# Performance work log

Hardware: AMD Instinct MI355X
Metric: run time of the kernel (lower is better)

Reference implementation:

```python
import jax, jax.numpy as jnp
import numpy as np

B, N, C_IN, C_OUT, CHEB_K, EMBED = 64, 2048, 64, 64, 3, 16


def setup_inputs() -> dict:
    key = jax.random.key(0)
    k1, k2, k3, k4 = jax.random.split(key, 4)
    return {
        "graph": 0,  # unused placeholder, matches original signature
        "node_feature": jax.random.normal(k1, (B, N, C_IN), dtype=jnp.float32),
        "node_embeddings": jax.random.normal(k2, (N, EMBED), dtype=jnp.float32),
        "weights_pool": jax.random.normal(k3, (EMBED, CHEB_K, C_IN, C_OUT), dtype=jnp.float32),
        "bias_pool": jax.random.normal(k4, (EMBED, C_OUT), dtype=jnp.float32),
    }


def reference(graph, node_feature, node_embeddings, weights_pool, bias_pool):
    x = node_feature                      # [B, N, C]
    n = node_embeddings.shape[0]
    # adaptive adjacency: softmax(relu(E E^T)) row-wise
    supports = jax.nn.softmax(jax.nn.relu(node_embeddings @ node_embeddings.T), axis=1)  # [N, N]
    # Chebyshev polynomial basis
    support_set = [jnp.eye(n, dtype=supports.dtype), supports]
    for _ in range(2, CHEB_K):
        support_set.append(2.0 * supports @ support_set[-1] - support_set[-2])
    supports_k = jnp.stack(support_set, axis=0)  # [K, N, N]
    # per-node dynamic weights / bias
    weights = jnp.einsum('nd,dkio->nkio', node_embeddings, weights_pool)  # [N, K, I, O]
    bias = node_embeddings @ bias_pool                                    # [N, O]
    # graph aggregation over Chebyshev orders
    x_g = jnp.einsum('knm,bmc->bnkc', supports_k, x)                      # [B, N, K, C]
    # per-node weighted contraction
    out = jnp.einsum('bnki,nkio->bno', x_g, weights) + bias               # [B, N, O]
    return out
```

## Files before the change

kernel.cpp:

```cpp
#include <hip/hip_runtime.h>
#include <hip/hip_bf16.h>

#define BB 64
#define NN 2048
#define CC 64
#define DD 16

typedef __attribute__((ext_vector_type(8))) short bf16x8;
typedef __attribute__((ext_vector_type(4))) float f32x4;

__device__ __forceinline__ ushort f2bf(float f) {
  unsigned u = __float_as_uint(f);
  u += 0x7fffu + ((u >> 16) & 1u);
  return (ushort)(u >> 16);
}
__device__ __forceinline__ float b2f(ushort h) {
  return __uint_as_float(((unsigned)h) << 16);
}

#define GLOAD16(g, l)                                                 \
  __builtin_amdgcn_global_load_lds(                                   \
      (const __attribute__((address_space(1))) void*)(g),             \
      (__attribute__((address_space(3))) void*)(l), 16, 0, 0)

__global__ __launch_bounds__(256) void transpose_x_kernel(
    const float* __restrict__ X, ushort* __restrict__ Xt) {
  const int b = blockIdx.y;
  const int m0 = blockIdx.x * 256;
  const int t = threadIdx.x;
  __shared__ ushort xs[256 * 64];

#pragma unroll
  for (int it = 0; it < 16; ++it) {
    const int idx = it * 256 + t;
    const int m = idx >> 4;
    const int cq = (idx & 15) * 4;
    float4 v = *(const float4*)&X[(size_t)b * NN * CC + (size_t)(m0 + m) * CC + cq];
    ushort4 h;
    h.x = f2bf(v.x); h.y = f2bf(v.y); h.z = f2bf(v.z); h.w = f2bf(v.w);
    *(ushort4*)((char*)xs + m * 128 + ((cq * 2) ^ ((m & 7) << 4))) = h;
  }
  __syncthreads();

  const int c = t >> 2;
  const int mb = (t & 3) * 64;
#pragma unroll
  for (int s = 0; s < 8; ++s) {
    unsigned w0 = 0, w1 = 0, w2 = 0, w3 = 0;
#pragma unroll
    for (int j = 0; j < 8; ++j) {
      const int m = mb + s * 8 + j;
      const ushort hv =
          *(const ushort*)((const char*)xs + m * 128 + ((2 * c) ^ ((m & 7) << 4)));
      const unsigned uv = (unsigned)hv << ((j & 1) * 16);
      if (j < 2) w0 |= uv; else if (j < 4) w1 |= uv;
      else if (j < 6) w2 |= uv; else w3 |= uv;
    }
    uint4 pk = {w0, w1, w2, w3};
    *(uint4*)&Xt[(size_t)b * CC * NN + (size_t)c * NN + m0 + mb + s * 8] = pk;
  }
}

__global__ __launch_bounds__(256) void wpt_kernel(
    const float* __restrict__ Wp, ushort* __restrict__ Wpt) {
  const int g = blockIdx.x * 256 + threadIdx.x;
  const int d = g / 1536;
  const int rem = g % 1536;
  const int o = rem / 24;
  const int ki0 = (rem % 24) * 8;
  bf16x8 h;
#pragma unroll
  for (int j = 0; j < 8; ++j)
    h[j] = (short)f2bf(Wp[d * 12288 + (ki0 + j) * 64 + o]);
  *(bf16x8*)&Wpt[d * 12288 + o * 192 + ki0] = h;
}

__global__ __launch_bounds__(256) void supports_kernel(
    const float* __restrict__ E, ushort* __restrict__ S) {
  const int n = blockIdx.x;
  const int t = threadIdx.x;

  __shared__ float en[DD];
  if (t < DD) en[t] = E[n * DD + t];
  __syncthreads();

  float e[DD];
#pragma unroll
  for (int d = 0; d < DD; ++d) e[d] = en[d];

  float vals[8];
  float vmax = 0.f;
#pragma unroll
  for (int j = 0; j < 8; ++j) {
    const int m = j * 256 + t;
    const float4* Em = (const float4*)&E[m * DD];
    float4 v0 = Em[0], v1 = Em[1], v2 = Em[2], v3 = Em[3];
    float dot = e[0]*v0.x + e[1]*v0.y + e[2]*v0.z + e[3]*v0.w
              + e[4]*v1.x + e[5]*v1.y + e[6]*v1.z + e[7]*v1.w
              + e[8]*v2.x + e[9]*v2.y + e[10]*v2.z + e[11]*v2.w
              + e[12]*v3.x + e[13]*v3.y + e[14]*v3.z + e[15]*v3.w;
    dot = fmaxf(dot, 0.f);
    vals[j] = dot;
    vmax = fmaxf(vmax, dot);
  }

  __shared__ float red[256];
  red[t] = vmax;
  __syncthreads();
  for (int s = 128; s > 0; s >>= 1) {
    if (t < s) red[t] = fmaxf(red[t], red[t + s]);
    __syncthreads();
  }
  vmax = red[0];
  __syncthreads();

  float sum = 0.f;
#pragma unroll
  for (int j = 0; j < 8; ++j) {
    vals[j] = __expf(vals[j] - vmax);
    sum += vals[j];
  }
  red[t] = sum;
  __syncthreads();
  for (int s = 128; s > 0; s >>= 1) {
    if (t < s) red[t] += red[t + s];
    __syncthreads();
  }
  const float inv = 1.f / red[0];

#pragma unroll
  for (int j = 0; j < 8; ++j)
    S[(size_t)n * NN + j * 256 + t] = f2bf(vals[j] * inv);
}

__global__ __launch_bounds__(256) void spmm_t_kernel(
    const ushort* __restrict__ At, const ushort* __restrict__ S,
    ushort* __restrict__ Yt, ushort* __restrict__ Yn) {
  const int b  = blockIdx.x;
  const int n0 = blockIdx.y * 256;
  const int t  = threadIdx.x;
  const int w  = t >> 6;
  const int l  = t & 63;

  __shared__ ushort Als[64 * 64];
  __shared__ ushort Bls[256 * 64];

  const char* Abase = (const char*)(At + (size_t)b * CC * NN);
  const char* Sbase = (const char*)S + (size_t)n0 * (NN * 2);

  f32x4 acc[4][4];
#pragma unroll
  for (int i = 0; i < 4; ++i)
#pragma unroll
    for (int j = 0; j < 4; ++j) acc[i][j] = (f32x4)0.f;

  const int lkb = (l & 7) * 16;
  const int lrw = w * 8 + (l >> 3);

  for (int mt = 0; mt < NN; mt += 64) {
    __syncthreads();
#pragma unroll
    for (int q = 0; q < 2; ++q) {
      const int row = q * 32 + lrw;
      GLOAD16(Abase + (size_t)row * (NN * 2) + mt * 2 + (lkb ^ ((row & 7) << 4)),
              (char*)Als + q * 4096 + w * 1024);
    }
#pragma unroll
    for (int q = 0; q < 8; ++q) {
      const int row = q * 32 + lrw;
      GLOAD16(Sbase + (size_t)row * (NN * 2) + mt * 2 + (lkb ^ ((row & 7) << 4)),
              (char*)Bls + q * 4096 + w * 1024);
    }
    __syncthreads();

#pragma unroll
    for (int kk = 0; kk < 2; ++kk) {
      const int kb = kk * 64 + (l >> 4) * 16;
      bf16x8 a[4], bv[4];
#pragma unroll
      for (int cf = 0; cf < 4; ++cf) {
        const int c = cf * 16 + (l & 15);
        a[cf] = *(const bf16x8*)((const char*)Als + c * 128 + (kb ^ ((c & 7) << 4)));
      }
#pragma unroll
      for (int nf = 0; nf < 4; ++nf) {
        const int r = w * 64 + nf * 16 + (l & 15);
        bv[nf] = *(const bf16x8*)((const char*)Bls + r * 128 + (kb ^ ((r & 7) << 4)));
      }
#pragma unroll
      for (int cf = 0; cf < 4; ++cf)
#pragma unroll
        for (int nf = 0; nf < 4; ++nf)
          acc[cf][nf] = __builtin_amdgcn_mfma_f32_16x16x32_bf16(
              a[cf], bv[nf], acc[cf][nf], 0, 0, 0);
    }
  }

  const int nw = n0 + w * 64;
#pragma unroll
  for (int cf = 0; cf < 4; ++cf) {
#pragma unroll
    for (int nf = 0; nf < 4; ++nf) {
      const int n = nw + nf * 16 + (l & 15);
      const int cb = cf * 16 + (l >> 4) * 4;
      ushort h0 = f2bf(acc[cf][nf][0]);
      ushort h1 = f2bf(acc[cf][nf][1]);
      ushort h2 = f2bf(acc[cf][nf][2]);
      ushort h3 = f2bf(acc[cf][nf][3]);
      if (Yt) {
        ushort* p = Yt + (size_t)b * CC * NN + (size_t)cb * NN + n;
        p[0] = h0; p[NN] = h1; p[2 * NN] = h2; p[3 * NN] = h3;
      }
      if (Yn) {
        ushort4 pk = {h0, h1, h2, h3};
        *(ushort4*)(Yn + (size_t)b * NN * CC + (size_t)n * CC + cb) = pk;
      }
    }
  }
}

__global__ __launch_bounds__(256) void out_kernel(
    const float* __restrict__ E, const ushort* __restrict__ Wpt,
    const float* __restrict__ Bp, const float* __restrict__ X,
    const ushort* __restrict__ Y1n, const ushort* __restrict__ Y1t,
    const ushort* __restrict__ Y2n, float* __restrict__ Out) {
  const int n = blockIdx.x;
  const int t = threadIdx.x;
  const int w = t >> 6, l = t & 63;

  __shared__ ushort Wt[64 * 192];
  __shared__ ushort xg[64 * 192];
  __shared__ float bsh[64];
  __shared__ float esh[DD];

  if (t < DD) esh[t] = E[n * DD + t];
  __syncthreads();
  float e[DD];
#pragma unroll
  for (int d = 0; d < DD; ++d) e[d] = esh[d];

  if (t < 64) {
    float bsum = 0.f;
#pragma unroll
    for (int d = 0; d < DD; ++d) bsum = fmaf(e[d], Bp[d * 64 + t], bsum);
    bsh[t] = bsum;
  }

#pragma unroll
  for (int it = 0; it < 6; ++it) {
    const int boff = it * 4096 + t * 16;
    float acc[8] = {};
#pragma unroll
    for (int d = 0; d < DD; ++d) {
      bf16x8 wv = *(const bf16x8*)((const char*)Wpt + d * 24576 + boff);
#pragma unroll
      for (int u = 0; u < 8; ++u)
        acc[u] = fmaf(e[d], b2f((ushort)wv[u]), acc[u]);
    }
    bf16x8 hv;
#pragma unroll
    for (int u = 0; u < 8; ++u) hv[u] = (short)f2bf(acc[u]);
    const int o = boff / 384;
    const int kib = boff % 384;
    *(bf16x8*)((char*)Wt + o * 384 + (kib ^ ((o & 7) << 4))) = hv;
  }

  {
    const int b = t >> 2, i0 = (t & 3) * 16;
    const size_t NC = (size_t)NN * CC;
    const size_t gbase = (size_t)b * NC + (size_t)n * CC + i0;
    float xv[16];
#pragma unroll
    for (int j = 0; j < 4; ++j) {
      float4 v = *(const float4*)&X[gbase + j * 4];
      xv[j * 4 + 0] = v.x; xv[j * 4 + 1] = v.y;
      xv[j * 4 + 2] = v.z; xv[j * 4 + 3] = v.w;
    }
#pragma unroll
    for (int h = 0; h < 2; ++h) {
      bf16x8 hv;
#pragma unroll
      for (int u = 0; u < 8; ++u) hv[u] = (short)f2bf(xv[h * 8 + u]);
      const int ki = i0 + h * 8;
      *(bf16x8*)((char*)xg + b * 384 + ((ki * 2) ^ ((b & 7) << 4))) = hv;
    }
    if (Y1n) {
#pragma unroll
      for (int h = 0; h < 2; ++h) {
        bf16x8 hv = *(const bf16x8*)&Y1n[gbase + h * 8];
        const int ki = 64 + i0 + h * 8;
        *(bf16x8*)((char*)xg + b * 384 + ((ki * 2) ^ ((b & 7) << 4))) = hv;
      }
    } else {
#pragma unroll
      for (int h = 0; h < 2; ++h) {
        bf16x8 hv;
#pragma unroll
        for (int u = 0; u < 8; ++u)
          hv[u] = (short)Y1t[(size_t)b * NC + (size_t)(i0 + h * 8 + u) * NN + n];
        const int ki = 64 + i0 + h * 8;
        *(bf16x8*)((char*)xg + b * 384 + ((ki * 2) ^ ((b & 7) << 4))) = hv;
      }
    }
#pragma unroll
    for (int h = 0; h < 2; ++h) {
      bf16x8 y2 = *(const bf16x8*)&Y2n[gbase + h * 8];
      bf16x8 hv;
#pragma unroll
      for (int u = 0; u < 8; ++u)
        hv[u] = (short)f2bf(2.f * b2f((ushort)y2[u]) - xv[h * 8 + u]);
      const int ki = 128 + i0 + h * 8;
      *(bf16x8*)((char*)xg + b * 384 + ((ki * 2) ^ ((b & 7) << 4))) = hv;
    }
  }
  __syncthreads();

  const int br = (w & 1) * 32, oc = (w >> 1) * 32;
  f32x4 acc[2][2];
#pragma unroll
  for (int i = 0; i < 2; ++i)
#pragma unroll
    for (int j = 0; j < 2; ++j) acc[i][j] = (f32x4)0.f;

#pragma unroll
  for (int s = 0; s < 6; ++s) {
    const int kb = s * 64 + (l >> 4) * 16;
    bf16x8 av[2], bv[2];
#pragma unroll
    for (int i = 0; i < 2; ++i) {
      const int row = br + i * 16 + (l & 15);
      av[i] = *(const bf16x8*)((const char*)xg + row * 384 + (kb ^ ((row & 7) << 4)));
    }
#pragma unroll
    for (int j = 0; j < 2; ++j) {
      const int row = oc + j * 16 + (l & 15);
      bv[j] = *(const bf16x8*)((const char*)Wt + row * 384 + (kb ^ ((row & 7) << 4)));
    }
#pragma unroll
    for (int i = 0; i < 2; ++i)
#pragma unroll
      for (int j = 0; j < 2; ++j)
        acc[i][j] = __builtin_amdgcn_mfma_f32_16x16x32_bf16(av[i], bv[j],
                                                            acc[i][j], 0, 0, 0);
  }

  const size_t NC = (size_t)NN * CC;
#pragma unroll
  for (int i = 0; i < 2; ++i) {
#pragma unroll
    for (int j = 0; j < 2; ++j) {
      const int o = oc + j * 16 + (l & 15);
      const int bb = br + i * 16 + (l >> 4) * 4;
      const float bo = bsh[o];
#pragma unroll
      for (int r = 0; r < 4; ++r)
        Out[(size_t)(bb + r) * NC + (size_t)n * CC + o] = acc[i][j][r] + bo;
    }
  }
}

extern "C" void kernel_launch(void* const* d_in, const int* in_sizes, int n_in,
                              void* d_out, int out_size, void* d_ws, size_t ws_size,
                              hipStream_t stream) {
  const float* x  = (const float*)d_in[1];
  const float* E  = (const float*)d_in[2];
  const float* Wp = (const float*)d_in[3];
  const float* Bp = (const float*)d_in[4];
  float* out = (float*)d_out;

  const size_t szS  = (size_t)NN * NN * 2;
  const size_t szY  = (size_t)BB * NN * CC * 2;
  const size_t szWp = (size_t)DD * 3 * CC * CC * 2;
  ushort* Sb  = (ushort*)d_ws;
  ushort* Xt  = (ushort*)((char*)d_ws + szS);
  ushort* Y1t = (ushort*)((char*)d_ws + szS + szY);
  ushort* Wpt = (ushort*)((char*)d_ws + szS + 2 * szY);
  ushort* Y1n = (ushort*)((char*)d_ws + szS + 2 * szY + szWp);
  ushort* Y2n = Xt;
  const bool haveY1n = ws_size >= szS + 3 * szY + szWp;

  transpose_x_kernel<<<dim3(NN / 256, BB), 256, 0, stream>>>(x, Xt);
  wpt_kernel<<<96, 256, 0, stream>>>(Wp, Wpt);
  supports_kernel<<<NN, 256, 0, stream>>>(E, Sb);

  dim3 g2(BB, NN / 256);
  spmm_t_kernel<<<g2, 256, 0, stream>>>(Xt, Sb, Y1t, haveY1n ? Y1n : nullptr);
  spmm_t_kernel<<<g2, 256, 0, stream>>>(Y1t, Sb, nullptr, Y2n);

  out_kernel<<<NN, 256, 0, stream>>>(E, Wpt, Bp, x, haveY1n ? Y1n : nullptr,
                                     Y1t, Y2n, out);
}
```

Before: 178.9 us.

## Double-buffer SpMM LDS tiles and process two nodes per output block

```diff
diff --git a/kernel.cpp b/kernel.cpp
--- a/kernel.cpp
+++ b/kernel.cpp
@@ -142,8 +142,8 @@
   const int w  = t >> 6;
   const int l  = t & 63;
 
-  __shared__ ushort Als[64 * 64];
-  __shared__ ushort Bls[256 * 64];
+  __shared__ ushort Als[2][64 * 64];
+  __shared__ ushort Bls[2][256 * 64];
 
   const char* Abase = (const char*)(At + (size_t)b * CC * NN);
   const char* Sbase = (const char*)S + (size_t)n0 * (NN * 2);
@@ -157,21 +157,29 @@
   const int lkb = (l & 7) * 16;
   const int lrw = w * 8 + (l >> 3);
 
-  for (int mt = 0; mt < NN; mt += 64) {
-    __syncthreads();
+  auto stage = [&](int buf, int mt) {
 #pragma unroll
     for (int q = 0; q < 2; ++q) {
       const int row = q * 32 + lrw;
       GLOAD16(Abase + (size_t)row * (NN * 2) + mt * 2 + (lkb ^ ((row & 7) << 4)),
-              (char*)Als + q * 4096 + w * 1024);
+              (char*)Als[buf] + q * 4096 + w * 1024);
     }
 #pragma unroll
     for (int q = 0; q < 8; ++q) {
       const int row = q * 32 + lrw;
       GLOAD16(Sbase + (size_t)row * (NN * 2) + mt * 2 + (lkb ^ ((row & 7) << 4)),
-              (char*)Bls + q * 4096 + w * 1024);
-    }
-    __syncthreads();
+              (char*)Bls[buf] + q * 4096 + w * 1024);
+    }
+  };
+
+  stage(0, 0);
+  int cur = 0;
+  for (int it = 0; it < 32; ++it) {
+    const int nmt = ((it + 1) & 31) * 64;
+    stage(cur ^ 1, nmt);
+    asm volatile("s_waitcnt vmcnt(10)" ::: "memory");
+    __builtin_amdgcn_s_barrier();
+    __builtin_amdgcn_sched_barrier(0);
 
 #pragma unroll
     for (int kk = 0; kk < 2; ++kk) {
@@ -180,12 +188,14 @@
 #pragma unroll
       for (int cf = 0; cf < 4; ++cf) {
         const int c = cf * 16 + (l & 15);
-        a[cf] = *(const bf16x8*)((const char*)Als + c * 128 + (kb ^ ((c & 7) << 4)));
+        a[cf] = *(const bf16x8*)((const char*)Als[cur] + c * 128 +
+                                 (kb ^ ((c & 7) << 4)));
       }
 #pragma unroll
       for (int nf = 0; nf < 4; ++nf) {
         const int r = w * 64 + nf * 16 + (l & 15);
-        bv[nf] = *(const bf16x8*)((const char*)Bls + r * 128 + (kb ^ ((r & 7) << 4)));
+        bv[nf] = *(const bf16x8*)((const char*)Bls[cur] + r * 128 +
+                                  (kb ^ ((r & 7) << 4)));
       }
 #pragma unroll
       for (int cf = 0; cf < 4; ++cf)
@@ -194,6 +204,10 @@
           acc[cf][nf] = __builtin_amdgcn_mfma_f32_16x16x32_bf16(
               a[cf], bv[nf], acc[cf][nf], 0, 0, 0);
     }
+
+    __builtin_amdgcn_sched_barrier(0);
+    __builtin_amdgcn_s_barrier();
+    cur ^= 1;
   }
 
   const int nw = n0 + w * 64;
@@ -219,56 +233,67 @@
   }
 }
 
-__global__ __launch_bounds__(256) void out_kernel(
+__global__ __launch_bounds__(512) void out_kernel(
     const float* __restrict__ E, const ushort* __restrict__ Wpt,
     const float* __restrict__ Bp, const float* __restrict__ X,
     const ushort* __restrict__ Y1n, const ushort* __restrict__ Y1t,
     const ushort* __restrict__ Y2n, float* __restrict__ Out) {
-  const int n = blockIdx.x;
+  const int n0 = blockIdx.x * 2;
   const int t = threadIdx.x;
-  const int w = t >> 6, l = t & 63;
-
-  __shared__ ushort Wt[64 * 192];
-  __shared__ ushort xg[64 * 192];
-  __shared__ float bsh[64];
-  __shared__ float esh[DD];
-
-  if (t < DD) esh[t] = E[n * DD + t];
-  __syncthreads();
-  float e[DD];
-#pragma unroll
-  for (int d = 0; d < DD; ++d) e[d] = esh[d];
-
-  if (t < 64) {
+
+  __shared__ ushort Wt[2][64 * 192];
+  __shared__ ushort xg[2][64 * 192];
+  __shared__ float bsh[2][64];
+  __shared__ float esh[2][DD];
+
+  if (t < 2 * DD) esh[t >> 4][t & 15] = E[(n0 + (t >> 4)) * DD + (t & 15)];
+  __syncthreads();
+  float ea[DD], eb[DD];
+#pragma unroll
+  for (int d = 0; d < DD; ++d) { ea[d] = esh[0][d]; eb[d] = esh[1][d]; }
+
+  if (t < 128) {
+    const int node = t >> 6, o = t & 63;
+    const float* e = node ? eb : ea;
     float bsum = 0.f;
 #pragma unroll
-    for (int d = 0; d < DD; ++d) bsum = fmaf(e[d], Bp[d * 64 + t], bsum);
-    bsh[t] = bsum;
-  }
-
-#pragma unroll
-  for (int it = 0; it < 6; ++it) {
-    const int boff = it * 4096 + t * 16;
-    float acc[8] = {};
+    for (int d = 0; d < DD; ++d) bsum = fmaf(e[d], Bp[d * 64 + o], bsum);
+    bsh[node][o] = bsum;
+  }
+
+#pragma unroll
+  for (int it = 0; it < 3; ++it) {
+    const int boff = it * 8192 + t * 16;
+    float acc0[8] = {}, acc1[8] = {};
 #pragma unroll
     for (int d = 0; d < DD; ++d) {
       bf16x8 wv = *(const bf16x8*)((const char*)Wpt + d * 24576 + boff);
 #pragma unroll
-      for (int u = 0; u < 8; ++u)
-        acc[u] = fmaf(e[d], b2f((ushort)wv[u]), acc[u]);
-    }
-    bf16x8 hv;
-#pragma unroll
-    for (int u = 0; u < 8; ++u) hv[u] = (short)f2bf(acc[u]);
+      for (int u = 0; u < 8; ++u) {
+        const float f = b2f((ushort)wv[u]);
+        acc0[u] = fmaf(ea[d], f, acc0[u]);
+        acc1[u] = fmaf(eb[d], f, acc1[u]);
+      }
+    }
+    bf16x8 h0, h1;
+#pragma unroll
+    for (int u = 0; u < 8; ++u) {
+      h0[u] = (short)f2bf(acc0[u]);
+      h1[u] = (short)f2bf(acc1[u]);
+    }
     const int o = boff / 384;
-    const int kib = boff % 384;
-    *(bf16x8*)((char*)Wt + o * 384 + (kib ^ ((o & 7) << 4))) = hv;
+    const int sw = (boff % 384) ^ ((o & 7) << 4);
+    *(bf16x8*)((char*)Wt[0] + o * 384 + sw) = h0;
+    *(bf16x8*)((char*)Wt[1] + o * 384 + sw) = h1;
   }
 
   {
-    const int b = t >> 2, i0 = (t & 3) * 16;
+    const int node = t >> 8, tt = t & 255;
+    const int b = tt >> 2, i0 = (tt & 3) * 16;
+    const int n = n0 + node;
     const size_t NC = (size_t)NN * CC;
     const size_t gbase = (size_t)b * NC + (size_t)n * CC + i0;
+    char* xgn = (char*)xg[node];
     float xv[16];
 #pragma unroll
     for (int j = 0; j < 4; ++j) {
@@ -282,14 +307,14 @@
 #pragma unroll
       for (int u = 0; u < 8; ++u) hv[u] = (short)f2bf(xv[h * 8 + u]);
       const int ki = i0 + h * 8;
-      *(bf16x8*)((char*)xg + b * 384 + ((ki * 2) ^ ((b & 7) << 4))) = hv;
+      *(bf16x8*)(xgn + b * 384 + ((ki * 2) ^ ((b & 7) << 4))) = hv;
     }
     if (Y1n) {
 #pragma unroll
       for (int h = 0; h < 2; ++h) {
         bf16x8 hv = *(const bf16x8*)&Y1n[gbase + h * 8];
         const int ki = 64 + i0 + h * 8;
-        *(bf16x8*)((char*)xg + b * 384 + ((ki * 2) ^ ((b & 7) << 4))) = hv;
+        *(bf16x8*)(xgn + b * 384 + ((ki * 2) ^ ((b & 7) << 4))) = hv;
       }
     } else {
 #pragma unroll
@@ -299,7 +324,7 @@
         for (int u = 0; u < 8; ++u)
           hv[u] = (short)Y1t[(size_t)b * NC + (size_t)(i0 + h * 8 + u) * NN + n];
         const int ki = 64 + i0 + h * 8;
-        *(bf16x8*)((char*)xg + b * 384 + ((ki * 2) ^ ((b & 7) << 4))) = hv;
+        *(bf16x8*)(xgn + b * 384 + ((ki * 2) ^ ((b & 7) << 4))) = hv;
       }
     }
 #pragma unroll
@@ -310,12 +335,17 @@
       for (int u = 0; u < 8; ++u)
         hv[u] = (short)f2bf(2.f * b2f((ushort)y2[u]) - xv[h * 8 + u]);
       const int ki = 128 + i0 + h * 8;
-      *(bf16x8*)((char*)xg + b * 384 + ((ki * 2) ^ ((b & 7) << 4))) = hv;
-    }
-  }
-  __syncthreads();
-
-  const int br = (w & 1) * 32, oc = (w >> 1) * 32;
+      *(bf16x8*)(xgn + b * 384 + ((ki * 2) ^ ((b & 7) << 4))) = hv;
+    }
+  }
+  __syncthreads();
+
+  const int w8 = t >> 6, l = t & 63;
+  const int node = w8 >> 2, q = w8 & 3;
+  const int br = (q & 1) * 32, oc = (q >> 1) * 32;
+  const char* xgn = (const char*)xg[node];
+  const char* wtn = (const char*)Wt[node];
+
   f32x4 acc[2][2];
 #pragma unroll
   for (int i = 0; i < 2; ++i)
@@ -329,12 +359,12 @@
 #pragma unroll
     for (int i = 0; i < 2; ++i) {
       const int row = br + i * 16 + (l & 15);
-      av[i] = *(const bf16x8*)((const char*)xg + row * 384 + (kb ^ ((row & 7) << 4)));
+      av[i] = *(const bf16x8*)(xgn + row * 384 + (kb ^ ((row & 7) << 4)));
     }
 #pragma unroll
     for (int j = 0; j < 2; ++j) {
       const int row = oc + j * 16 + (l & 15);
-      bv[j] = *(const bf16x8*)((const char*)Wt + row * 384 + (kb ^ ((row & 7) << 4)));
+      bv[j] = *(const bf16x8*)(wtn + row * 384 + (kb ^ ((row & 7) << 4)));
     }
 #pragma unroll
     for (int i = 0; i < 2; ++i)
@@ -345,13 +375,14 @@
   }
 
   const size_t NC = (size_t)NN * CC;
+  const int n = n0 + node;
 #pragma unroll
   for (int i = 0; i < 2; ++i) {
 #pragma unroll
     for (int j = 0; j < 2; ++j) {
       const int o = oc + j * 16 + (l & 15);
       const int bb = br + i * 16 + (l >> 4) * 4;
-      const float bo = bsh[o];
+      const float bo = bsh[node][o];
 #pragma unroll
       for (int r = 0; r < 4; ++r)
         Out[(size_t)(bb + r) * NC + (size_t)n * CC + o] = acc[i][j][r] + bo;
@@ -387,6 +418,6 @@
   spmm_t_kernel<<<g2, 256, 0, stream>>>(Xt, Sb, Y1t, haveY1n ? Y1n : nullptr);
   spmm_t_kernel<<<g2, 256, 0, stream>>>(Y1t, Sb, nullptr, Y2n);
 
-  out_kernel<<<NN, 256, 0, stream>>>(E, Wpt, Bp, x, haveY1n ? Y1n : nullptr,
-                                     Y1t, Y2n, out);
-}
+  out_kernel<<<NN / 2, 512, 0, stream>>>(E, Wpt, Bp, x, haveY1n ? Y1n : nullptr,
+                                         Y1t, Y2n, out);
+}
```

Result: faster. 172.8 us, median of 3 (-3.4%).
